# Kernel optimization log

Measured on AMD Instinct MI355X. Metric: run time of the kernel, lower is better.

## Reference

```python
import jax, jax.numpy as jnp
from jax import lax
import numpy as np

VOCAB, EMB, SEQ, HID, BATCH = 50000, 300, 80, 128, 4096


def setup_inputs() -> dict:
    key = jax.random.key(0)
    ks = jax.random.split(key, 7)
    x = jax.random.randint(ks[0], (BATCH, SEQ), 0, VOCAB)
    emb = jax.random.normal(ks[1], (VOCAB, EMB), jnp.float32) * 0.05  # frozen pretrained table
    # Keras SimpleRNN: kernel (glorot), recurrent_kernel (orthogonal-ish), bias zeros
    Wxh = jax.random.normal(ks[2], (EMB, HID), jnp.float32) * (1.0 / np.sqrt(EMB))
    Whh = jax.random.normal(ks[3], (HID, HID), jnp.float32) * (1.0 / np.sqrt(HID))
    bh = jnp.zeros((HID,), jnp.float32)
    Wd = jax.random.normal(ks[4], (HID, 1), jnp.float32) * (1.0 / np.sqrt(HID))
    bd = jnp.zeros((1,), jnp.float32)
    return {"x": x, "emb": emb, "Wxh": Wxh, "Whh": Whh, "bh": bh, "Wd": Wd, "bd": bd}


def reference(x, emb, Wxh, Whh, bh, Wd, bd):
    # Embedding lookup: [B, T] -> [B, T, E]
    e = emb[x]
    # Precompute input projection for all timesteps: [B, T, H]
    xp = jnp.einsum('bte,eh->bth', e, Wxh) + bh
    # SimpleRNN recurrence (tanh), return only last hidden state
    def step(h, xt):  # xt: [B, H]
        h = jnp.tanh(xt + h @ Whh)
        return h, None
    h0 = jnp.zeros((x.shape[0], Whh.shape[0]), xp.dtype)
    h_last, _ = lax.scan(step, h0, jnp.swapaxes(xp, 0, 1))  # scan over time
    # Dense(1, sigmoid): [B, 1]
    return jax.nn.sigmoid(h_last @ Wd + bd)
```

## Files before the change

kernel.cpp:

```cpp
#include <hip/hip_runtime.h>
#include <hip/hip_fp16.h>
#include <cstdint>

#define VOCAB 50000
#define EMB   300
#define EMBP  320
#define SEQ   80
#define HID   128
#define BATCH 4096
#define ROWS  16
#define THREADS 512

typedef __attribute__((ext_vector_type(8))) _Float16 f16x8;
typedef __attribute__((ext_vector_type(4))) float    f32x4;

static __device__ __forceinline__ float fast_tanh(float xv) {
    const float e = __expf(2.f * xv);
    return 1.f - 2.f / (e + 1.f);
}
static __device__ __forceinline__ float f16b2f(unsigned short u) {
    _Float16 h;
    __builtin_memcpy(&h, &u, 2);
    return (float)h;
}

__global__ __launch_bounds__(256) void k_embcvt(const float* __restrict__ emb,
                                                _Float16* __restrict__ out) {
    const int gid = blockIdx.x * 256 + threadIdx.x;
    if (gid >= VOCAB * (EMBP / 4)) return;
    const int r  = gid / (EMBP / 4);
    const int c4 = gid % (EMBP / 4);
    ushort4 o; o.x = o.y = o.z = o.w = 0;
    if (c4 < EMB / 4) {
        const float4 v = *reinterpret_cast<const float4*>(emb + (size_t)r * EMB + c4 * 4);
        _Float16 a = (_Float16)v.x, b = (_Float16)v.y,
                 c = (_Float16)v.z, d = (_Float16)v.w;
        o.x = *(unsigned short*)&a; o.y = *(unsigned short*)&b;
        o.z = *(unsigned short*)&c; o.w = *(unsigned short*)&d;
    }
    *reinterpret_cast<ushort4*>((unsigned short*)out + (size_t)r * EMBP + c4 * 4) = o;
}

__global__ __launch_bounds__(THREADS, 2) void k_fused(
    const int*      __restrict__ x,
    const _Float16* __restrict__ embb,
    const float*    __restrict__ Wxh,
    const float*    __restrict__ Whh,
    const float*    __restrict__ bh,
    const float*    __restrict__ Wd,
    const float*    __restrict__ bd,
    float*          __restrict__ out)
{
    __shared__ __align__(16) unsigned char Abuf[2][ROWS * EMBP * 2];
    __shared__ __align__(16) unsigned char Hbuf[2][ROWS * HID * 2];
    __shared__ int xidx[ROWS * SEQ];

    const int tid  = threadIdx.x;
    const int lane = tid & 63;
    const int wv   = tid >> 6;
    const int r16  = lane & 15;
    const int g    = lane >> 4;
    const int rb   = blockIdx.x * ROWS;

    for (int q = tid; q < ROWS * SEQ; q += THREADS) xidx[q] = x[rb * SEQ + q];
    if (tid < 256) {
        uint4 z = {};
        *reinterpret_cast<uint4*>(&Hbuf[0][tid * 16]) = z;
    }

    const int col = 16 * wv + r16;

    int a_off[10], h_off[4], w_off[4];
    #pragma unroll
    for (int ks = 0; ks < 10; ++ks)
        a_off[ks] = r16 * 640 + (((4 * ks + g) ^ (r16 & 7)) * 16);
    #pragma unroll
    for (int ks = 0; ks < 4; ++ks)
        h_off[ks] = r16 * 256 + (((4 * ks + g) ^ r16) * 16);
    #pragma unroll
    for (int r = 0; r < 4; ++r) {
        const int rr = 4 * g + r;
        w_off[r] = rr * 256 + (((col >> 3) ^ rr) * 16) + (col & 7) * 2;
    }

    f16x8 wx[10];
    #pragma unroll
    for (int ks = 0; ks < 10; ++ks) {
        f16x8 f;
        #pragma unroll
        for (int j = 0; j < 8; ++j) {
            const int kk = 32 * ks + 8 * g + j;
            f[j] = (_Float16)(kk < EMB ? Wxh[kk * HID + col] : 0.f);
        }
        wx[ks] = f;
    }
    f16x8 wh[4];
    #pragma unroll
    for (int ks = 0; ks < 4; ++ks) {
        f16x8 f;
        #pragma unroll
        for (int j = 0; j < 8; ++j) {
            const int kk = 32 * ks + 8 * g + j;
            f[j] = (_Float16)Whh[kk * HID + col];
        }
        wh[ks] = f;
    }
    const float bhv = bh[col];

    const int  q0 = tid;
    const bool on1 = (tid < 128);
    const int  q1 = on1 ? (tid + 512) : 0;
    const int grow0 = q0 / 40, goff0 = q0 % 40;
    const int grow1 = q1 / 40, goff1 = q1 % 40;
    const int ldst0 = grow0 * 640 + ((goff0 ^ (grow0 & 7)) * 16);
    const int ldst1 = grow1 * 640 + ((goff1 ^ (grow1 & 7)) * 16);

    char* const hb0 = (char*)&Hbuf[0][0];

    __syncthreads();

    {
        const uint4 t0 = *reinterpret_cast<const uint4*>(
            (const unsigned short*)embb + (size_t)xidx[grow0 * SEQ] * EMBP + goff0 * 8);
        *reinterpret_cast<uint4*>(&Abuf[0][ldst0]) = t0;
        if (on1) {
            const uint4 t1 = *reinterpret_cast<const uint4*>(
                (const unsigned short*)embb + (size_t)xidx[grow1 * SEQ] * EMBP + goff1 * 8);
            *reinterpret_cast<uint4*>(&Abuf[0][ldst1]) = t1;
        }
    }
    uint4 cur0, cur1 = {}, nxt0 = {}, nxt1 = {};
    cur0 = *reinterpret_cast<const uint4*>(
        (const unsigned short*)embb + (size_t)xidx[grow0 * SEQ + 1] * EMBP + goff0 * 8);
    if (on1) cur1 = *reinterpret_cast<const uint4*>(
        (const unsigned short*)embb + (size_t)xidx[grow1 * SEQ + 1] * EMBP + goff1 * 8);

    asm volatile("s_waitcnt lgkmcnt(0)" ::: "memory");
    __builtin_amdgcn_s_barrier();
    __builtin_amdgcn_sched_barrier(0);

    const f32x4 z4 = {0.f, 0.f, 0.f, 0.f};

#define STEP(T, P, CUR0, CUR1, NXT0, NXT1)                                         \
    {                                                                              \
                        \
        if ((T) + 1 < SEQ) {                                                       \
            *reinterpret_cast<uint4*>(&Abuf[(P) ^ 1][ldst0]) = CUR0;               \
            if (on1) *reinterpret_cast<uint4*>(&Abuf[(P) ^ 1][ldst1]) = CUR1;      \
        }                                                                          \
                                           \
        if ((T) + 2 < SEQ) {                                                       \
            NXT0 = *reinterpret_cast<const uint4*>((const unsigned short*)embb +   \
                (size_t)xidx[grow0 * SEQ + (T) + 2] * EMBP + goff0 * 8);           \
            if (on1) NXT1 = *reinterpret_cast<const uint4*>(                       \
                (const unsigned short*)embb +                                      \
                (size_t)xidx[grow1 * SEQ + (T) + 2] * EMBP + goff1 * 8);           \
        }                                                                          \
                                       \
        const unsigned char* ab = &Abuf[P][0];                                     \
        const unsigned char* hb = &Hbuf[P][0];                                     \
        f32x4 accA = z4, accB = z4;                                                \
        _Pragma("unroll")                                                          \
        for (int ks = 0; ks < 10; ks += 2) {                                       \
            const f16x8 aeA = *reinterpret_cast<const f16x8*>(ab + a_off[ks]);     \
            const f16x8 aeB = *reinterpret_cast<const f16x8*>(ab + a_off[ks + 1]); \
            accA = __builtin_amdgcn_mfma_f32_16x16x32_f16(aeA, wx[ks], accA,0,0,0);\
            accB = __builtin_amdgcn_mfma_f32_16x16x32_f16(aeB, wx[ks+1],accB,0,0,0);\
        }                                                                          \
        const f16x8 h0 = *reinterpret_cast<const f16x8*>(hb + h_off[0]);           \
        const f16x8 h1 = *reinterpret_cast<const f16x8*>(hb + h_off[1]);           \
        const f16x8 h2 = *reinterpret_cast<const f16x8*>(hb + h_off[2]);           \
        const f16x8 h3 = *reinterpret_cast<const f16x8*>(hb + h_off[3]);           \
        accA = __builtin_amdgcn_mfma_f32_16x16x32_f16(h0, wh[0], accA, 0, 0, 0);   \
        accB = __builtin_amdgcn_mfma_f32_16x16x32_f16(h1, wh[1], accB, 0, 0, 0);   \
        accA = __builtin_amdgcn_mfma_f32_16x16x32_f16(h2, wh[2], accA, 0, 0, 0);   \
        accB = __builtin_amdgcn_mfma_f32_16x16x32_f16(h3, wh[3], accB, 0, 0, 0);   \
                                                            \
        unsigned char* hw = &Hbuf[(P) ^ 1][0];                                     \
        _Pragma("unroll")                                                          \
        for (int r = 0; r < 4; ++r) {                                              \
            const float v = fast_tanh(accA[r] + accB[r] + bhv);                    \
            *reinterpret_cast<_Float16*>(hw + w_off[r]) = (_Float16)v;             \
        }                                                                          \
        asm volatile("s_waitcnt lgkmcnt(0)" ::: "memory");                         \
        __builtin_amdgcn_s_barrier();                                              \
        __builtin_amdgcn_sched_barrier(0);                                         \
    }

    for (int t = 0; t < SEQ; t += 2) {
        STEP(t,     0, cur0, cur1, nxt0, nxt1);
        STEP(t + 1, 1, nxt0, nxt1, cur0, cur1);
    }
#undef STEP

    const int r = tid >> 5;
    const int m = tid & 31;
    const int base = r * 256 + ((((m >> 1)) ^ r) * 16) + ((4 * m) & 7) * 2;
    const ushort4 hu = *reinterpret_cast<const ushort4*>(hb0 + base);
    const float4  wd = *reinterpret_cast<const float4*>(&Wd[4 * m]);
    float part = f16b2f(hu.x) * wd.x + f16b2f(hu.y) * wd.y
               + f16b2f(hu.z) * wd.z + f16b2f(hu.w) * wd.w;
    part += __shfl_down(part, 16, 32);
    part += __shfl_down(part, 8, 32);
    part += __shfl_down(part, 4, 32);
    part += __shfl_down(part, 2, 32);
    part += __shfl_down(part, 1, 32);
    if (m == 0) out[rb + r] = 1.f / (1.f + expf(-(part + bd[0])));
}

extern "C" void kernel_launch(void* const* d_in, const int* in_sizes, int n_in,
                              void* d_out, int out_size, void* d_ws, size_t ws_size,
                              hipStream_t stream)
{
    (void)in_sizes; (void)n_in; (void)out_size; (void)ws_size;
    const int*   x   = (const int*)  d_in[0];
    const float* emb = (const float*)d_in[1];
    const float* Wxh = (const float*)d_in[2];
    const float* Whh = (const float*)d_in[3];
    const float* bh  = (const float*)d_in[4];
    const float* Wd  = (const float*)d_in[5];
    const float* bd  = (const float*)d_in[6];
    float* out = (float*)d_out;

    _Float16* embb = (_Float16*)d_ws;

    const int n_cvt = VOCAB * (EMBP / 4);
    k_embcvt<<<(n_cvt + 255) / 256, 256, 0, stream>>>(emb, embb);
    k_fused<<<BATCH / ROWS, THREADS, 0, stream>>>(x, embb, Wxh, Whh, bh, Wd, bd, out);
}
```

Before: 82.67 us.

## Precompute projected embedding table emb@Wxh and gather projections in RNN

Instead of converting the embedding table to fp16 and doing the input projection per token inside the recurrence, a first kernel computes P = emb @ Wxh for the whole vocabulary (50000x128, fp16). The RNN kernel then gathers 128-wide projected rows per token and seeds the accumulator with them, which removes 10 MFMAs per step and shrinks the gathered row from 320 to 128 halves. The trade is a vocabulary-sized GEMM per call, and the bias is still added in fp32 at tanh time.

```diff
diff --git a/kernel.cpp b/kernel.cpp
--- a/kernel.cpp
+++ b/kernel.cpp
@@ -4,12 +4,10 @@
 
 #define VOCAB 50000
 #define EMB   300
-#define EMBP  320
 #define SEQ   80
 #define HID   128
 #define BATCH 4096
 #define ROWS  16
-#define THREADS 512
 
 typedef __attribute__((ext_vector_type(8))) _Float16 f16x8;
 typedef __attribute__((ext_vector_type(4))) float    f32x4;
@@ -23,64 +21,47 @@
     __builtin_memcpy(&h, &u, 2);
     return (float)h;
 }
-
-__global__ __launch_bounds__(256) void k_embcvt(const float* __restrict__ emb,
-                                                _Float16* __restrict__ out) {
-    const int gid = blockIdx.x * 256 + threadIdx.x;
-    if (gid >= VOCAB * (EMBP / 4)) return;
-    const int r  = gid / (EMBP / 4);
-    const int c4 = gid % (EMBP / 4);
-    ushort4 o; o.x = o.y = o.z = o.w = 0;
-    if (c4 < EMB / 4) {
-        const float4 v = *reinterpret_cast<const float4*>(emb + (size_t)r * EMB + c4 * 4);
-        _Float16 a = (_Float16)v.x, b = (_Float16)v.y,
-                 c = (_Float16)v.z, d = (_Float16)v.w;
-        o.x = *(unsigned short*)&a; o.y = *(unsigned short*)&b;
-        o.z = *(unsigned short*)&c; o.w = *(unsigned short*)&d;
-    }
-    *reinterpret_cast<ushort4*>((unsigned short*)out + (size_t)r * EMBP + c4 * 4) = o;
-}
-
-__global__ __launch_bounds__(THREADS, 2) void k_fused(
-    const int*      __restrict__ x,
-    const _Float16* __restrict__ embb,
-    const float*    __restrict__ Wxh,
-    const float*    __restrict__ Whh,
-    const float*    __restrict__ bh,
-    const float*    __restrict__ Wd,
-    const float*    __restrict__ bd,
-    float*          __restrict__ out)
+static __device__ __forceinline__ unsigned pack2h(float a, float b) {
+    _Float16 ha = (_Float16)a, hb = (_Float16)b;
+    unsigned short ua, ub;
+    __builtin_memcpy(&ua, &ha, 2);
+    __builtin_memcpy(&ub, &hb, 2);
+    return (unsigned)ua | ((unsigned)ub << 16);
+}
+
+__global__ __launch_bounds__(512, 2) void k_ptab(
+    const float* __restrict__ emb,
+    const float* __restrict__ Wxh,
+    _Float16*    __restrict__ P)
 {
-    __shared__ __align__(16) unsigned char Abuf[2][ROWS * EMBP * 2];
-    __shared__ __align__(16) unsigned char Hbuf[2][ROWS * HID * 2];
-    __shared__ int xidx[ROWS * SEQ];
+    __shared__ __align__(16) unsigned char As[ROWS * 640];
+    __shared__ __align__(16) _Float16 Ps[ROWS][HID];
 
     const int tid  = threadIdx.x;
     const int lane = tid & 63;
     const int wv   = tid >> 6;
     const int r16  = lane & 15;
     const int g    = lane >> 4;
-    const int rb   = blockIdx.x * ROWS;
-
-    for (int q = tid; q < ROWS * SEQ; q += THREADS) xidx[q] = x[rb * SEQ + q];
-    if (tid < 256) {
-        uint4 z = {};
-        *reinterpret_cast<uint4*>(&Hbuf[0][tid * 16]) = z;
-    }
-
-    const int col = 16 * wv + r16;
-
-    int a_off[10], h_off[4], w_off[4];
-    #pragma unroll
-    for (int ks = 0; ks < 10; ++ks)
-        a_off[ks] = r16 * 640 + (((4 * ks + g) ^ (r16 & 7)) * 16);
-    #pragma unroll
-    for (int ks = 0; ks < 4; ++ks)
-        h_off[ks] = r16 * 256 + (((4 * ks + g) ^ r16) * 16);
-    #pragma unroll
-    for (int r = 0; r < 4; ++r) {
-        const int rr = 4 * g + r;
-        w_off[r] = rr * 256 + (((col >> 3) ^ rr) * 16) + (col & 7) * 2;
+    const int v0   = blockIdx.x * ROWS;
+    const int col  = 16 * wv + r16;
+
+    for (int q = tid; q < ROWS * 40; q += 512) {
+        const int row = q / 40, f = q % 40;
+        const float* src = emb + (size_t)(v0 + row) * EMB + 8 * f;
+        float va[8] = {0.f, 0.f, 0.f, 0.f, 0.f, 0.f, 0.f, 0.f};
+        if (f <= 36) {
+            const float4 u0 = *reinterpret_cast<const float4*>(src);
+            const float4 u1 = *reinterpret_cast<const float4*>(src + 4);
+            va[0] = u0.x; va[1] = u0.y; va[2] = u0.z; va[3] = u0.w;
+            va[4] = u1.x; va[5] = u1.y; va[6] = u1.z; va[7] = u1.w;
+        } else if (f == 37) {
+            const float4 u0 = *reinterpret_cast<const float4*>(src);
+            va[0] = u0.x; va[1] = u0.y; va[2] = u0.z; va[3] = u0.w;
+        }
+        uint4 o;
+        o.x = pack2h(va[0], va[1]); o.y = pack2h(va[2], va[3]);
+        o.z = pack2h(va[4], va[5]); o.w = pack2h(va[6], va[7]);
+        *reinterpret_cast<uint4*>(&As[row * 640 + ((f ^ (row & 7)) * 16)]) = o;
     }
 
     f16x8 wx[10];
@@ -94,46 +75,97 @@
         }
         wx[ks] = f;
     }
+    __syncthreads();
+
+    const f32x4 z4 = {0.f, 0.f, 0.f, 0.f};
+    f32x4 accA = z4, accB = z4;
+    #pragma unroll
+    for (int ks = 0; ks < 10; ks += 2) {
+        const f16x8 aA = *reinterpret_cast<const f16x8*>(
+            &As[r16 * 640 + (((4 * ks + g) ^ (r16 & 7)) * 16)]);
+        const f16x8 aB = *reinterpret_cast<const f16x8*>(
+            &As[r16 * 640 + (((4 * (ks + 1) + g) ^ (r16 & 7)) * 16)]);
+        accA = __builtin_amdgcn_mfma_f32_16x16x32_f16(aA, wx[ks],     accA, 0, 0, 0);
+        accB = __builtin_amdgcn_mfma_f32_16x16x32_f16(aB, wx[ks + 1], accB, 0, 0, 0);
+    }
+    #pragma unroll
+    for (int r = 0; r < 4; ++r)
+        Ps[4 * g + r][col] = (_Float16)(accA[r] + accB[r]);
+    __syncthreads();
+
+    if (tid < 256) {
+        const int row = tid >> 4, k = tid & 15;
+        *reinterpret_cast<uint4*>(P + (size_t)(v0 + row) * HID + 8 * k) =
+            *reinterpret_cast<const uint4*>(&Ps[row][8 * k]);
+    }
+}
+
+__global__ __launch_bounds__(512, 2) void k_rnn(
+    const int*      __restrict__ x,
+    const _Float16* __restrict__ P,
+    const float*    __restrict__ Whh,
+    const float*    __restrict__ bh,
+    const float*    __restrict__ Wd,
+    const float*    __restrict__ bd,
+    float*          __restrict__ out)
+{
+    __shared__ __align__(16) unsigned char Xbuf[2][ROWS * HID * 2];
+    __shared__ __align__(16) unsigned char Hbuf[2][ROWS * HID * 2];
+    __shared__ int xidx[ROWS * SEQ];
+
+    const int tid  = threadIdx.x;
+    const int lane = tid & 63;
+    const int wv   = tid >> 6;
+    const int r16  = lane & 15;
+    const int g    = lane >> 4;
+    const int rb   = blockIdx.x * ROWS;
+
+    for (int q = tid; q < ROWS * SEQ; q += 512) xidx[q] = x[rb * SEQ + q];
+    if (tid < 256) {
+        uint4 z = {};
+        *reinterpret_cast<uint4*>(&Hbuf[0][tid * 16]) = z;
+    }
+
+    const int col = 16 * wv + r16;
+
+    int h_off[4], w_off[4], x_off[4];
+    #pragma unroll
+    for (int ks = 0; ks < 4; ++ks)
+        h_off[ks] = r16 * 256 + (((4 * ks + g) ^ r16) * 16);
+    #pragma unroll
+    for (int r = 0; r < 4; ++r) {
+        const int rr = 4 * g + r;
+        w_off[r] = rr * 256 + (((col >> 3) ^ rr) * 16) + (col & 7) * 2;
+        x_off[r] = (wv * 512 + g * 128 + r * 32 + r16 * 2) ^ (((wv + g) & 3) << 4);
+    }
+
     f16x8 wh[4];
     #pragma unroll
     for (int ks = 0; ks < 4; ++ks) {
         f16x8 f;
         #pragma unroll
-        for (int j = 0; j < 8; ++j) {
-            const int kk = 32 * ks + 8 * g + j;
-            f[j] = (_Float16)Whh[kk * HID + col];
-        }
+        for (int j = 0; j < 8; ++j)
+            f[j] = (_Float16)Whh[(32 * ks + 8 * g + j) * HID + col];
         wh[ks] = f;
     }
     const float bhv = bh[col];
 
-    const int  q0 = tid;
-    const bool on1 = (tid < 128);
-    const int  q1 = on1 ? (tid + 512) : 0;
-    const int grow0 = q0 / 40, goff0 = q0 % 40;
-    const int grow1 = q1 / 40, goff1 = q1 % 40;
-    const int ldst0 = grow0 * 640 + ((goff0 ^ (grow0 & 7)) * 16);
-    const int ldst1 = grow1 * 640 + ((goff1 ^ (grow1 & 7)) * 16);
-
-    char* const hb0 = (char*)&Hbuf[0][0];
+    const bool gon  = (tid < 256);
+    const int  grow = (tid & 255) >> 4;
+    const int  gk   = tid & 15;
+    const int  gdst = ((gk >> 1) * 512 + (grow >> 2) * 128 + (grow & 3) * 32 +
+                       (gk & 1) * 16) ^ ((((gk >> 1) + (grow >> 2)) & 3) << 4);
 
     __syncthreads();
 
-    {
+    if (gon) {
         const uint4 t0 = *reinterpret_cast<const uint4*>(
-            (const unsigned short*)embb + (size_t)xidx[grow0 * SEQ] * EMBP + goff0 * 8);
-        *reinterpret_cast<uint4*>(&Abuf[0][ldst0]) = t0;
-        if (on1) {
-            const uint4 t1 = *reinterpret_cast<const uint4*>(
-                (const unsigned short*)embb + (size_t)xidx[grow1 * SEQ] * EMBP + goff1 * 8);
-            *reinterpret_cast<uint4*>(&Abuf[0][ldst1]) = t1;
-        }
-    }
-    uint4 cur0, cur1 = {}, nxt0 = {}, nxt1 = {};
-    cur0 = *reinterpret_cast<const uint4*>(
-        (const unsigned short*)embb + (size_t)xidx[grow0 * SEQ + 1] * EMBP + goff0 * 8);
-    if (on1) cur1 = *reinterpret_cast<const uint4*>(
-        (const unsigned short*)embb + (size_t)xidx[grow1 * SEQ + 1] * EMBP + goff1 * 8);
+            P + (size_t)xidx[grow * SEQ] * HID + 8 * gk);
+        *reinterpret_cast<uint4*>(&Xbuf[0][gdst]) = t0;
+    }
+    uint4 cur = {}, nxt = {};
+    if (gon) cur = *reinterpret_cast<const uint4*>(
+        P + (size_t)xidx[grow * SEQ + 1] * HID + 8 * gk);
 
     asm volatile("s_waitcnt lgkmcnt(0)" ::: "memory");
     __builtin_amdgcn_s_barrier();
@@ -141,32 +173,23 @@
 
     const f32x4 z4 = {0.f, 0.f, 0.f, 0.f};
 
-#define STEP(T, P, CUR0, CUR1, NXT0, NXT1)                                         \
+#define STEP(T, PB, CUR, NXT)                                                      \
     {                                                                              \
-                        \
-        if ((T) + 1 < SEQ) {                                                       \
-            *reinterpret_cast<uint4*>(&Abuf[(P) ^ 1][ldst0]) = CUR0;               \
-            if (on1) *reinterpret_cast<uint4*>(&Abuf[(P) ^ 1][ldst1]) = CUR1;      \
-        }                                                                          \
-                                           \
-        if ((T) + 2 < SEQ) {                                                       \
-            NXT0 = *reinterpret_cast<const uint4*>((const unsigned short*)embb +   \
-                (size_t)xidx[grow0 * SEQ + (T) + 2] * EMBP + goff0 * 8);           \
-            if (on1) NXT1 = *reinterpret_cast<const uint4*>(                       \
-                (const unsigned short*)embb +                                      \
-                (size_t)xidx[grow1 * SEQ + (T) + 2] * EMBP + goff1 * 8);           \
-        }                                                                          \
-                                       \
-        const unsigned char* ab = &Abuf[P][0];                                     \
-        const unsigned char* hb = &Hbuf[P][0];                                     \
-        f32x4 accA = z4, accB = z4;                                                \
+                         \
+        if ((T) + 1 < SEQ && gon)                                                  \
+            *reinterpret_cast<uint4*>(&Xbuf[(PB) ^ 1][gdst]) = CUR;                \
+                                                  \
+        if ((T) + 2 < SEQ && gon)                                                  \
+            NXT = *reinterpret_cast<const uint4*>(                                 \
+                P + (size_t)xidx[grow * SEQ + (T) + 2] * HID + 8 * gk);            \
+               \
+        const unsigned char* xb = &Xbuf[PB][0];                                    \
+        const unsigned char* hb = &Hbuf[PB][0];                                    \
+        f32x4 accA, accB = z4;                                                     \
         _Pragma("unroll")                                                          \
-        for (int ks = 0; ks < 10; ks += 2) {                                       \
-            const f16x8 aeA = *reinterpret_cast<const f16x8*>(ab + a_off[ks]);     \
-            const f16x8 aeB = *reinterpret_cast<const f16x8*>(ab + a_off[ks + 1]); \
-            accA = __builtin_amdgcn_mfma_f32_16x16x32_f16(aeA, wx[ks], accA,0,0,0);\
-            accB = __builtin_amdgcn_mfma_f32_16x16x32_f16(aeB, wx[ks+1],accB,0,0,0);\
-        }                                                                          \
+        for (int r = 0; r < 4; ++r)                                                \
+            accA[r] = f16b2f(*reinterpret_cast<const unsigned short*>(             \
+                xb + x_off[r]));                                                   \
         const f16x8 h0 = *reinterpret_cast<const f16x8*>(hb + h_off[0]);           \
         const f16x8 h1 = *reinterpret_cast<const f16x8*>(hb + h_off[1]);           \
         const f16x8 h2 = *reinterpret_cast<const f16x8*>(hb + h_off[2]);           \
@@ -175,8 +198,7 @@
         accB = __builtin_amdgcn_mfma_f32_16x16x32_f16(h1, wh[1], accB, 0, 0, 0);   \
         accA = __builtin_amdgcn_mfma_f32_16x16x32_f16(h2, wh[2], accA, 0, 0, 0);   \
         accB = __builtin_amdgcn_mfma_f32_16x16x32_f16(h3, wh[3], accB, 0, 0, 0);   \
-                                                            \
-        unsigned char* hw = &Hbuf[(P) ^ 1][0];                                     \
+        unsigned char* hw = &Hbuf[(PB) ^ 1][0];                                    \
         _Pragma("unroll")                                                          \
         for (int r = 0; r < 4; ++r) {                                              \
             const float v = fast_tanh(accA[r] + accB[r] + bhv);                    \
@@ -188,14 +210,15 @@
     }
 
     for (int t = 0; t < SEQ; t += 2) {
-        STEP(t,     0, cur0, cur1, nxt0, nxt1);
-        STEP(t + 1, 1, nxt0, nxt1, cur0, cur1);
+        STEP(t,     0, cur, nxt);
+        STEP(t + 1, 1, nxt, cur);
     }
 #undef STEP
 
+    const char* hb0 = (const char*)&Hbuf[0][0];
     const int r = tid >> 5;
     const int m = tid & 31;
-    const int base = r * 256 + ((((m >> 1)) ^ r) * 16) + ((4 * m) & 7) * 2;
+    const int base = r * 256 + (((m >> 1)) ^ r) * 16 + ((4 * m) & 7) * 2;
     const ushort4 hu = *reinterpret_cast<const ushort4*>(hb0 + base);
     const float4  wd = *reinterpret_cast<const float4*>(&Wd[4 * m]);
     float part = f16b2f(hu.x) * wd.x + f16b2f(hu.y) * wd.y
@@ -222,9 +245,8 @@
     const float* bd  = (const float*)d_in[6];
     float* out = (float*)d_out;
 
-    _Float16* embb = (_Float16*)d_ws;
-
-    const int n_cvt = VOCAB * (EMBP / 4);
-    k_embcvt<<<(n_cvt + 255) / 256, 256, 0, stream>>>(emb, embb);
-    k_fused<<<BATCH / ROWS, THREADS, 0, stream>>>(x, embb, Wxh, Whh, bh, Wd, bd, out);
-}
+    _Float16* P = (_Float16*)d_ws;
+
+    k_ptab<<<VOCAB / ROWS, 512, 0, stream>>>(emb, Wxh, P);
+    k_rnn<<<BATCH / ROWS, 512, 0, stream>>>(x, P, Whh, bh, Wd, bd, out);
+}
```

After: 90.68 us. +9.7%, slower.
